# Optimization experiments

Measured on AMD Instinct MI355X. Metric: run time of the kernel, lower is better.

The kernel has to match this reference:

```python
import jax, jax.numpy as jnp
import numpy as np

EPS = 1e-3  # BatchNorm eps from module init
N, C_IN, K = 200000, 256, 27
C_MID = C_IN // 4  # bottleneck expansion = 4


def batch_norm(h, gamma, beta):
    # BatchNorm1d in training mode: biased batch stats over the node dim
    mean = jnp.mean(h, axis=0)
    var = jnp.var(h, axis=0)
    return (h - mean) * jax.lax.rsqrt(var + EPS) * gamma + beta


def setup_inputs() -> dict:
    key = jax.random.key(0)
    ks = jax.random.split(key, 8)
    x = jax.random.normal(ks[0], (N, C_IN), dtype=jnp.float32)
    neigh = jax.random.randint(ks[1], (N, K), 0, N)  # 27-neighbor octree table
    # conv weights (no bias; BN follows). Fan-in scaled init.
    W1 = jax.random.normal(ks[2], (C_IN, C_MID), dtype=jnp.float32) / np.sqrt(C_IN)
    W2 = jax.random.normal(ks[3], (K, C_MID, C_MID), dtype=jnp.float32) / np.sqrt(K * C_MID)
    W3 = jax.random.normal(ks[4], (C_MID, C_IN), dtype=jnp.float32) / np.sqrt(C_MID)
    g1 = jnp.ones((C_MID,), jnp.float32); b1 = jnp.zeros((C_MID,), jnp.float32)
    g2 = jnp.ones((C_MID,), jnp.float32); b2 = jnp.zeros((C_MID,), jnp.float32)
    g3 = jnp.ones((C_IN,), jnp.float32); b3 = jnp.zeros((C_IN,), jnp.float32)
    return {"x": x, "neigh": neigh, "depth": 6,
            "W1": W1, "g1": g1, "b1": b1,
            "W2": W2, "g2": g2, "b2": b2,
            "W3": W3, "g3": g3, "b3": b3}


def reference(x, neigh, depth, W1, g1, b1, W2, g2, b2, W3, g3, b3):
    identity = x
    # conv_bn_relu1: 1x1 octree conv -> BN -> ReLU
    h = jax.nn.relu(batch_norm(x @ W1, g1, b1))  # [N, C_MID]
    # conv_bn_relu2: 3x3 octree conv (27-neighbor gather) -> BN -> ReLU
    gathered = h[neigh]                          # [N, 27, C_MID] irregular gather
    h = jnp.einsum('nkc,kcd->nd', gathered, W2)  # [N, C_MID]
    h = jax.nn.relu(batch_norm(h, g2, b2))
    # conv3: 1x1 octree conv back to C_IN, then BN + residual + ReLU
    h = batch_norm(h @ W3, g3, b3)               # [N, C_IN]
    return jax.nn.relu(h + identity)
```

## Files before the change

kernel.cpp:

```cpp
#include <hip/hip_runtime.h>
#include <stdint.h>

#define N_NODES 200000
#define C_INN   256
#define C_MIDD  64
#define KNB     27

typedef unsigned short u16;
typedef __attribute__((ext_vector_type(8))) short short8;
typedef __attribute__((ext_vector_type(4))) float floatx4;

__device__ inline float bf2f(u16 u) {
  union { uint32_t i; float f; } v; v.i = ((uint32_t)u) << 16; return v.f;
}
__device__ inline u16 f2bf(float f) {
  union { float f; uint32_t i; } v; v.f = f;
  uint32_t lsb = (v.i >> 16) & 1u;
  uint32_t r = v.i + 0x7fffu + lsb;
  return (u16)(r >> 16);
}

__global__ void prep_kernel(const float* __restrict__ W1, const float* __restrict__ W2,
                            const float* __restrict__ W3,
                            u16* __restrict__ w1t, u16* __restrict__ w2t,
                            u16* __restrict__ w3t, float* __restrict__ stats) {
  int tid = blockIdx.x * blockDim.x + threadIdx.x;
  int nth = gridDim.x * blockDim.x;
  for (int i = tid; i < 1536; i += nth) stats[i] = 0.f;
  for (int i = tid; i < 256 * 64; i += nth) {
    int d = i >> 8, k = i & 255;
    w1t[i] = f2bf(W1[k * 64 + d]);
  }
  for (int i = tid; i < 27 * 64 * 64; i += nth) {
    int kn = i >> 12, r = i & 4095, d = r >> 6, c = r & 63;
    w2t[i] = f2bf(W2[kn * 4096 + c * 64 + d]);
  }
  for (int i = tid; i < 256 * 64; i += nth) {
    int d = i >> 6, k = i & 63;
    w3t[i] = f2bf(W3[k * 256 + d]);
  }
}

#define PAD1 136
__global__ __launch_bounds__(256) void gemm1_kernel(const float* __restrict__ x,
                                                    const u16* __restrict__ w1t,
                                                    u16* __restrict__ y1) {
  __shared__ u16 Als[64 * PAD1];
  __shared__ u16 Bls[64 * PAD1];
  int t = threadIdx.x;
  long long rowBase = (long long)blockIdx.x * 64;
  int w = t >> 6, lane = t & 63;
  int m = lane & 15, q = lane >> 4;
  floatx4 acc[4] = {};

  for (int kh = 0; kh < 2; kh++) {
    if (kh) __syncthreads();
    #pragma unroll
    for (int j = 0; j < 8; j++) {
      int lin = j * 256 + t;
      int r = lin >> 5, c4 = lin & 31;
      floatx4 v = ((const floatx4*)x)[(rowBase + r) * 64 + kh * 32 + c4];
      ushort4 u;
      u.x = f2bf(v[0]); u.y = f2bf(v[1]); u.z = f2bf(v[2]); u.w = f2bf(v[3]);
      *(ushort4*)&Als[r * PAD1 + c4 * 4] = u;
    }
    #pragma unroll
    for (int j = 0; j < 4; j++) {
      int lin = j * 256 + t;
      int n = lin >> 4, c8 = lin & 15;
      uint4 u = ((const uint4*)w1t)[n * 32 + kh * 16 + c8];
      *(uint4*)&Bls[n * PAD1 + c8 * 8] = u;
    }
    __syncthreads();
    #pragma unroll
    for (int kc = 0; kc < 4; kc++) {
      short8 af = *(const short8*)&Als[(w * 16 + m) * PAD1 + kc * 32 + q * 8];
      #pragma unroll
      for (int tt = 0; tt < 4; tt++) {
        short8 bf = *(const short8*)&Bls[(tt * 16 + m) * PAD1 + kc * 32 + q * 8];
        acc[tt] = __builtin_amdgcn_mfma_f32_16x16x32_bf16(af, bf, acc[tt], 0, 0, 0);
      }
    }
  }
  long long base = rowBase + w * 16;
  #pragma unroll
  for (int tt = 0; tt < 4; tt++)
    #pragma unroll
    for (int r = 0; r < 4; r++)
      y1[(base + q * 4 + r) * 64 + tt * 16 + m] = f2bf(acc[tt][r]);
}

#define PAD2 72
__global__ __launch_bounds__(256) void gemm2_kernel(const u16* __restrict__ h1,
                                                    const int* __restrict__ neigh,
                                                    const u16* __restrict__ w2t,
                                                    u16* __restrict__ y2) {
  __shared__ u16 Als[64 * PAD2];
  __shared__ u16 Bls[64 * PAD2];
  __shared__ int nidx[64 * 27];
  int t = threadIdx.x;
  long long rowBase = (long long)blockIdx.x * 64;
  #pragma unroll
  for (int j = 0; j < 7; j++) {
    int lin = j * 256 + t;
    if (lin < 64 * 27) nidx[lin] = neigh[rowBase * 27 + lin];
  }
  int w = t >> 6, lane = t & 63;
  int m = lane & 15, q = lane >> 4;
  floatx4 acc[4] = {};

  for (int k = 0; k < KNB; k++) {
    __syncthreads();
    #pragma unroll
    for (int j = 0; j < 2; j++) {
      int lin = j * 256 + t;
      int r = lin >> 3, c8 = lin & 7;
      long long src = (long long)nidx[r * 27 + k] * 8 + c8;
      *(uint4*)&Als[r * PAD2 + c8 * 8] = ((const uint4*)h1)[src];
      *(uint4*)&Bls[r * PAD2 + c8 * 8] = ((const uint4*)w2t)[k * 512 + lin];
    }
    __syncthreads();
    #pragma unroll
    for (int kc = 0; kc < 2; kc++) {
      short8 af = *(const short8*)&Als[(w * 16 + m) * PAD2 + kc * 32 + q * 8];
      #pragma unroll
      for (int tt = 0; tt < 4; tt++) {
        short8 bf = *(const short8*)&Bls[(tt * 16 + m) * PAD2 + kc * 32 + q * 8];
        acc[tt] = __builtin_amdgcn_mfma_f32_16x16x32_bf16(af, bf, acc[tt], 0, 0, 0);
      }
    }
  }
  long long base = rowBase + w * 16;
  #pragma unroll
  for (int tt = 0; tt < 4; tt++)
    #pragma unroll
    for (int r = 0; r < 4; r++)
      y2[(base + q * 4 + r) * 64 + tt * 16 + m] = f2bf(acc[tt][r]);
}

#define PAD3 72
__global__ __launch_bounds__(256) void gemm3_kernel(const u16* __restrict__ h2,
                                                    const u16* __restrict__ w3t,
                                                    float* __restrict__ y3) {
  __shared__ u16 Als[64 * PAD3];
  __shared__ u16 Bls[256 * PAD3];
  int t = threadIdx.x;
  long long rowBase = (long long)blockIdx.x * 64;
  #pragma unroll
  for (int j = 0; j < 2; j++) {
    int lin = j * 256 + t;
    int r = lin >> 3, c8 = lin & 7;
    *(uint4*)&Als[r * PAD3 + c8 * 8] = ((const uint4*)h2)[rowBase * 8 + lin];
  }
  #pragma unroll
  for (int j = 0; j < 8; j++) {
    int lin = j * 256 + t;
    int n = lin >> 3, c8 = lin & 7;
    *(uint4*)&Bls[n * PAD3 + c8 * 8] = ((const uint4*)w3t)[lin];
  }
  __syncthreads();
  int w = t >> 6, lane = t & 63;
  int m = lane & 15, q = lane >> 4;
  floatx4 acc[16] = {};
  short8 af0 = *(const short8*)&Als[(w * 16 + m) * PAD3 + q * 8];
  short8 af1 = *(const short8*)&Als[(w * 16 + m) * PAD3 + 32 + q * 8];
  #pragma unroll
  for (int tt = 0; tt < 16; tt++) {
    short8 b0 = *(const short8*)&Bls[(tt * 16 + m) * PAD3 + q * 8];
    short8 b1 = *(const short8*)&Bls[(tt * 16 + m) * PAD3 + 32 + q * 8];
    acc[tt] = __builtin_amdgcn_mfma_f32_16x16x32_bf16(af0, b0, acc[tt], 0, 0, 0);
    acc[tt] = __builtin_amdgcn_mfma_f32_16x16x32_bf16(af1, b1, acc[tt], 0, 0, 0);
  }
  long long base = rowBase + w * 16;
  #pragma unroll
  for (int tt = 0; tt < 16; tt++)
    #pragma unroll
    for (int r = 0; r < 4; r++)
      y3[(base + q * 4 + r) * 256 + tt * 16 + m] = acc[tt][r];
}

template <int C, bool BF>
__global__ __launch_bounds__(256) void stats_kernel(const void* __restrict__ yv,
                                                    float* __restrict__ sums) {
  const int RPB = 256 / C;
  int t = threadIdx.x;
  int c = t % C, rg = t / C;
  float s = 0.f, sq = 0.f;
  for (long long row = (long long)blockIdx.x * RPB + rg; row < N_NODES;
       row += (long long)gridDim.x * RPB) {
    float v = BF ? bf2f(((const u16*)yv)[row * C + c])
                 : ((const float*)yv)[row * C + c];
    s += v; sq += v * v;
  }
  __shared__ float ls[256], lq[256];
  ls[t] = s; lq[t] = sq;
  __syncthreads();
  if (t < C) {
    float S = 0.f, Q = 0.f;
    for (int g = 0; g < RPB; g++) { S += ls[g * C + t]; Q += lq[g * C + t]; }
    atomicAdd(&sums[t], S);
    atomicAdd(&sums[C + t], Q);
  }
}

__global__ void finalize_kernel(const float* __restrict__ sums, const float* __restrict__ g,
                                const float* __restrict__ b, float* __restrict__ ac, int C) {
  int t = threadIdx.x;
  if (t < C) {
    float inv = 1.f / (float)N_NODES;
    float mean = sums[t] * inv;
    float var = sums[C + t] * inv - mean * mean;
    float a = g[t] * rsqrtf(var + 1e-3f);
    ac[t] = a;
    ac[C + t] = b[t] - mean * a;
  }
}

__global__ __launch_bounds__(256) void apply_bn_relu_kernel(u16* __restrict__ y,
                                                            const float* __restrict__ ac) {
  __shared__ float a[64], cc[64];
  int t = threadIdx.x;
  if (t < 64) { a[t] = ac[t]; cc[t] = ac[64 + t]; }
  __syncthreads();
  const long long total = (long long)N_NODES * 64 / 8;
  for (long long i = (long long)blockIdx.x * 256 + t; i < total;
       i += (long long)gridDim.x * 256) {
    uint4 u = ((uint4*)y)[i];
    int c0 = (int)((i & 7) * 8);
    u16* us = (u16*)&u;
    #pragma unroll
    for (int j = 0; j < 8; j++) {
      float v = bf2f(us[j]);
      v = fmaf(a[c0 + j], v, cc[c0 + j]);
      us[j] = f2bf(fmaxf(v, 0.f));
    }
    ((uint4*)y)[i] = u;
  }
}

__global__ __launch_bounds__(256) void epilogue_kernel(float* __restrict__ y3,
                                                       const float* __restrict__ x,
                                                       const float* __restrict__ ac) {
  __shared__ float a[256], cc[256];
  int t = threadIdx.x;
  a[t] = ac[t]; cc[t] = ac[256 + t];
  __syncthreads();
  const long long total = (long long)N_NODES * 256 / 4;
  for (long long i = (long long)blockIdx.x * 256 + t; i < total;
       i += (long long)gridDim.x * 256) {
    floatx4 v = ((floatx4*)y3)[i];
    floatx4 xi = ((const floatx4*)x)[i];
    int c0 = (int)((i & 63) * 4);
    #pragma unroll
    for (int j = 0; j < 4; j++) {
      float r = fmaf(a[c0 + j], v[j], cc[c0 + j]) + xi[j];
      v[j] = fmaxf(r, 0.f);
    }
    ((floatx4*)y3)[i] = v;
  }
}

extern "C" void kernel_launch(void* const* d_in, const int* in_sizes, int n_in,
                              void* d_out, int out_size, void* d_ws, size_t ws_size,
                              hipStream_t stream) {
  (void)in_sizes; (void)n_in; (void)out_size; (void)ws_size;
  const float* x  = (const float*)d_in[0];
  const int* neigh = (const int*)d_in[1];
  const float* W1 = (const float*)d_in[3];
  const float* g1 = (const float*)d_in[4];
  const float* b1 = (const float*)d_in[5];
  const float* W2 = (const float*)d_in[6];
  const float* g2 = (const float*)d_in[7];
  const float* b2 = (const float*)d_in[8];
  const float* W3 = (const float*)d_in[9];
  const float* g3 = (const float*)d_in[10];
  const float* b3 = (const float*)d_in[11];

  char* ws = (char*)d_ws;
  u16* h1  = (u16*)(ws);
  u16* h2  = (u16*)(ws + 25600000LL);
  u16* w1t = (u16*)(ws + 51200000LL);
  u16* w2t = (u16*)(ws + 51232768LL);
  u16* w3t = (u16*)(ws + 51453952LL);
  float* stats = (float*)(ws + 51486720LL);
  float* s1 = stats,        *ac1 = stats + 128;
  float* s2 = stats + 256,  *ac2 = stats + 384;
  float* s3 = stats + 512,  *ac3 = stats + 1024;
  float* y3 = (float*)d_out;

  const int MB = N_NODES / 64;

  prep_kernel<<<256, 256, 0, stream>>>(W1, W2, W3, w1t, w2t, w3t, stats);

  gemm1_kernel<<<MB, 256, 0, stream>>>(x, w1t, h1);
  stats_kernel<64, true><<<1024, 256, 0, stream>>>(h1, s1);
  finalize_kernel<<<1, 256, 0, stream>>>(s1, g1, b1, ac1, 64);
  apply_bn_relu_kernel<<<2048, 256, 0, stream>>>(h1, ac1);

  gemm2_kernel<<<MB, 256, 0, stream>>>(h1, neigh, w2t, h2);
  stats_kernel<64, true><<<1024, 256, 0, stream>>>(h2, s2);
  finalize_kernel<<<1, 256, 0, stream>>>(s2, g2, b2, ac2, 64);
  apply_bn_relu_kernel<<<2048, 256, 0, stream>>>(h2, ac2);

  gemm3_kernel<<<MB, 256, 0, stream>>>(h2, w3t, y3);
  stats_kernel<256, false><<<2048, 256, 0, stream>>>(y3, s3);
  finalize_kernel<<<1, 256, 0, stream>>>(s3, g3, b3, ac3, 256);
  epilogue_kernel<<<4096, 256, 0, stream>>>(y3, x, ac3);
}
```

Measured before the change: 768.8 us.

## Fuse BN stats into GEMMs, derive BN3 stats via Gram matrix, fuse epilogue

Batch statistics are now computed inside gemm1 and gemm2 epilogues, which removes the separate stats passes. BN3 statistics come from a 64x64 Gram matrix of the post-ReLU h2 multiplied through W3, so the fp32 y3 intermediate is never written or re-read. gemm3 applies BN2+ReLU on load and BN3, the residual and ReLU in its epilogue, writing the output once. gemm2 now takes 256-row tiles that read gathered rows directly from global memory instead of staging through LDS. The costs are a bf16-rounded Gram matrix for the variance, float atomics, and aliasing of G over the w1t workspace.

```diff
diff --git a/kernel.cpp b/kernel.cpp
--- a/kernel.cpp
+++ b/kernel.cpp
@@ -2,9 +2,6 @@
 #include <stdint.h>
 
 #define N_NODES 200000
-#define C_INN   256
-#define C_MIDD  64
-#define KNB     27
 
 typedef unsigned short u16;
 typedef __attribute__((ext_vector_type(8))) short short8;
@@ -16,196 +13,81 @@
 __device__ inline u16 f2bf(float f) {
   union { float f; uint32_t i; } v; v.f = f;
   uint32_t lsb = (v.i >> 16) & 1u;
-  uint32_t r = v.i + 0x7fffu + lsb;
-  return (u16)(r >> 16);
-}
+  return (u16)((v.i + 0x7fffu + lsb) >> 16);
+}
+
 
 __global__ void prep_kernel(const float* __restrict__ W1, const float* __restrict__ W2,
                             const float* __restrict__ W3,
                             u16* __restrict__ w1t, u16* __restrict__ w2t,
-                            u16* __restrict__ w3t, float* __restrict__ stats) {
+                            u16* __restrict__ w3t, float* __restrict__ fl) {
   int tid = blockIdx.x * blockDim.x + threadIdx.x;
   int nth = gridDim.x * blockDim.x;
-  for (int i = tid; i < 1536; i += nth) stats[i] = 0.f;
+  for (int i = tid; i < 512; i += nth) fl[i] = 0.f;
   for (int i = tid; i < 256 * 64; i += nth) {
-    int d = i >> 8, k = i & 255;
-    w1t[i] = f2bf(W1[k * 64 + d]);
+    int n = i >> 8, k = i & 255;
+    w1t[i] = f2bf(W1[k * 64 + n]);
   }
   for (int i = tid; i < 27 * 64 * 64; i += nth) {
-    int kn = i >> 12, r = i & 4095, d = r >> 6, c = r & 63;
-    w2t[i] = f2bf(W2[kn * 4096 + c * 64 + d]);
+    int kn = i >> 12, r = i & 4095, n = r >> 6, k = r & 63;
+    w2t[i] = f2bf(W2[kn * 4096 + k * 64 + n]);
   }
   for (int i = tid; i < 256 * 64; i += nth) {
-    int d = i >> 6, k = i & 63;
-    w3t[i] = f2bf(W3[k * 256 + d]);
-  }
-}
-
-#define PAD1 136
+    int n = i >> 6, k = i & 63;
+    w3t[i] = f2bf(W3[k * 256 + n]);
+  }
+}
+
 __global__ __launch_bounds__(256) void gemm1_kernel(const float* __restrict__ x,
                                                     const u16* __restrict__ w1t,
-                                                    u16* __restrict__ y1) {
-  __shared__ u16 Als[64 * PAD1];
-  __shared__ u16 Bls[64 * PAD1];
+                                                    u16* __restrict__ y1,
+                                                    float* __restrict__ s1) {
+  __shared__ float ps[4][64], pq[4][64];
+  int t = threadIdx.x, w = t >> 6, lane = t & 63, m = lane & 15, q = lane >> 4;
+  long long rowA = (long long)blockIdx.x * 64 + w * 16 + m;
+  const float* xr = x + rowA * 256 + q * 8;
+  floatx4 acc[4] = {};
+  #pragma unroll
+  for (int kc = 0; kc < 8; kc++) {
+    floatx4 v0 = *(const floatx4*)(xr + kc * 32);
+    floatx4 v1 = *(const floatx4*)(xr + kc * 32 + 4);
+    short8 af;
+    af[0] = f2bf(v0[0]); af[1] = f2bf(v0[1]); af[2] = f2bf(v0[2]); af[3] = f2bf(v0[3]);
+    af[4] = f2bf(v1[0]); af[5] = f2bf(v1[1]); af[6] = f2bf(v1[2]); af[7] = f2bf(v1[3]);
+    #pragma unroll
+    for (int tt = 0; tt < 4; tt++) {
+      short8 bf = *(const short8*)(w1t + (tt * 16 + m) * 256 + kc * 32 + q * 8);
+      acc[tt] = __builtin_amdgcn_mfma_f32_16x16x32_bf16(af, bf, acc[tt], 0, 0, 0);
+    }
+  }
+  long long rowC = (long long)blockIdx.x * 64 + w * 16 + q * 4;
+  #pragma unroll
+  for (int tt = 0; tt < 4; tt++) {
+    float s = 0.f, sq = 0.f;
+    #pragma unroll
+    for (int r = 0; r < 4; r++) {
+      float v = acc[tt][r];
+      s += v; sq += v * v;
+      y1[(rowC + r) * 64 + tt * 16 + m] = f2bf(v);
+    }
+    s += __shfl_xor(s, 16); s += __shfl_xor(s, 32);
+    sq += __shfl_xor(sq, 16); sq += __shfl_xor(sq, 32);
+    if (q == 0) { ps[w][tt * 16 + m] = s; pq[w][tt * 16 + m] = sq; }
+  }
+  __syncthreads();
+  if (t < 64) {
+    float S = ps[0][t] + ps[1][t] + ps[2][t] + ps[3][t];
+    float Q = pq[0][t] + pq[1][t] + pq[2][t] + pq[3][t];
+    atomicAdd(&s1[t], S);
+    atomicAdd(&s1[64 + t], Q);
+  }
+}
+
+__global__ void finalize_kernel(const float* __restrict__ sums, const float* __restrict__ g,
+                                const float* __restrict__ b, float* __restrict__ ac, int C,
+                                float* __restrict__ zp, int zn) {
   int t = threadIdx.x;
-  long long rowBase = (long long)blockIdx.x * 64;
-  int w = t >> 6, lane = t & 63;
-  int m = lane & 15, q = lane >> 4;
-  floatx4 acc[4] = {};
-
-  for (int kh = 0; kh < 2; kh++) {
-    if (kh) __syncthreads();
-    #pragma unroll
-    for (int j = 0; j < 8; j++) {
-      int lin = j * 256 + t;
-      int r = lin >> 5, c4 = lin & 31;
-      floatx4 v = ((const floatx4*)x)[(rowBase + r) * 64 + kh * 32 + c4];
-      ushort4 u;
-      u.x = f2bf(v[0]); u.y = f2bf(v[1]); u.z = f2bf(v[2]); u.w = f2bf(v[3]);
-      *(ushort4*)&Als[r * PAD1 + c4 * 4] = u;
-    }
-    #pragma unroll
-    for (int j = 0; j < 4; j++) {
-      int lin = j * 256 + t;
-      int n = lin >> 4, c8 = lin & 15;
-      uint4 u = ((const uint4*)w1t)[n * 32 + kh * 16 + c8];
-      *(uint4*)&Bls[n * PAD1 + c8 * 8] = u;
-    }
-    __syncthreads();
-    #pragma unroll
-    for (int kc = 0; kc < 4; kc++) {
-      short8 af = *(const short8*)&Als[(w * 16 + m) * PAD1 + kc * 32 + q * 8];
-      #pragma unroll
-      for (int tt = 0; tt < 4; tt++) {
-        short8 bf = *(const short8*)&Bls[(tt * 16 + m) * PAD1 + kc * 32 + q * 8];
-        acc[tt] = __builtin_amdgcn_mfma_f32_16x16x32_bf16(af, bf, acc[tt], 0, 0, 0);
-      }
-    }
-  }
-  long long base = rowBase + w * 16;
-  #pragma unroll
-  for (int tt = 0; tt < 4; tt++)
-    #pragma unroll
-    for (int r = 0; r < 4; r++)
-      y1[(base + q * 4 + r) * 64 + tt * 16 + m] = f2bf(acc[tt][r]);
-}
-
-#define PAD2 72
-__global__ __launch_bounds__(256) void gemm2_kernel(const u16* __restrict__ h1,
-                                                    const int* __restrict__ neigh,
-                                                    const u16* __restrict__ w2t,
-                                                    u16* __restrict__ y2) {
-  __shared__ u16 Als[64 * PAD2];
-  __shared__ u16 Bls[64 * PAD2];
-  __shared__ int nidx[64 * 27];
-  int t = threadIdx.x;
-  long long rowBase = (long long)blockIdx.x * 64;
-  #pragma unroll
-  for (int j = 0; j < 7; j++) {
-    int lin = j * 256 + t;
-    if (lin < 64 * 27) nidx[lin] = neigh[rowBase * 27 + lin];
-  }
-  int w = t >> 6, lane = t & 63;
-  int m = lane & 15, q = lane >> 4;
-  floatx4 acc[4] = {};
-
-  for (int k = 0; k < KNB; k++) {
-    __syncthreads();
-    #pragma unroll
-    for (int j = 0; j < 2; j++) {
-      int lin = j * 256 + t;
-      int r = lin >> 3, c8 = lin & 7;
-      long long src = (long long)nidx[r * 27 + k] * 8 + c8;
-      *(uint4*)&Als[r * PAD2 + c8 * 8] = ((const uint4*)h1)[src];
-      *(uint4*)&Bls[r * PAD2 + c8 * 8] = ((const uint4*)w2t)[k * 512 + lin];
-    }
-    __syncthreads();
-    #pragma unroll
-    for (int kc = 0; kc < 2; kc++) {
-      short8 af = *(const short8*)&Als[(w * 16 + m) * PAD2 + kc * 32 + q * 8];
-      #pragma unroll
-      for (int tt = 0; tt < 4; tt++) {
-        short8 bf = *(const short8*)&Bls[(tt * 16 + m) * PAD2 + kc * 32 + q * 8];
-        acc[tt] = __builtin_amdgcn_mfma_f32_16x16x32_bf16(af, bf, acc[tt], 0, 0, 0);
-      }
-    }
-  }
-  long long base = rowBase + w * 16;
-  #pragma unroll
-  for (int tt = 0; tt < 4; tt++)
-    #pragma unroll
-    for (int r = 0; r < 4; r++)
-      y2[(base + q * 4 + r) * 64 + tt * 16 + m] = f2bf(acc[tt][r]);
-}
-
-#define PAD3 72
-__global__ __launch_bounds__(256) void gemm3_kernel(const u16* __restrict__ h2,
-                                                    const u16* __restrict__ w3t,
-                                                    float* __restrict__ y3) {
-  __shared__ u16 Als[64 * PAD3];
-  __shared__ u16 Bls[256 * PAD3];
-  int t = threadIdx.x;
-  long long rowBase = (long long)blockIdx.x * 64;
-  #pragma unroll
-  for (int j = 0; j < 2; j++) {
-    int lin = j * 256 + t;
-    int r = lin >> 3, c8 = lin & 7;
-    *(uint4*)&Als[r * PAD3 + c8 * 8] = ((const uint4*)h2)[rowBase * 8 + lin];
-  }
-  #pragma unroll
-  for (int j = 0; j < 8; j++) {
-    int lin = j * 256 + t;
-    int n = lin >> 3, c8 = lin & 7;
-    *(uint4*)&Bls[n * PAD3 + c8 * 8] = ((const uint4*)w3t)[lin];
-  }
-  __syncthreads();
-  int w = t >> 6, lane = t & 63;
-  int m = lane & 15, q = lane >> 4;
-  floatx4 acc[16] = {};
-  short8 af0 = *(const short8*)&Als[(w * 16 + m) * PAD3 + q * 8];
-  short8 af1 = *(const short8*)&Als[(w * 16 + m) * PAD3 + 32 + q * 8];
-  #pragma unroll
-  for (int tt = 0; tt < 16; tt++) {
-    short8 b0 = *(const short8*)&Bls[(tt * 16 + m) * PAD3 + q * 8];
-    short8 b1 = *(const short8*)&Bls[(tt * 16 + m) * PAD3 + 32 + q * 8];
-    acc[tt] = __builtin_amdgcn_mfma_f32_16x16x32_bf16(af0, b0, acc[tt], 0, 0, 0);
-    acc[tt] = __builtin_amdgcn_mfma_f32_16x16x32_bf16(af1, b1, acc[tt], 0, 0, 0);
-  }
-  long long base = rowBase + w * 16;
-  #pragma unroll
-  for (int tt = 0; tt < 16; tt++)
-    #pragma unroll
-    for (int r = 0; r < 4; r++)
-      y3[(base + q * 4 + r) * 256 + tt * 16 + m] = acc[tt][r];
-}
-
-template <int C, bool BF>
-__global__ __launch_bounds__(256) void stats_kernel(const void* __restrict__ yv,
-                                                    float* __restrict__ sums) {
-  const int RPB = 256 / C;
-  int t = threadIdx.x;
-  int c = t % C, rg = t / C;
-  float s = 0.f, sq = 0.f;
-  for (long long row = (long long)blockIdx.x * RPB + rg; row < N_NODES;
-       row += (long long)gridDim.x * RPB) {
-    float v = BF ? bf2f(((const u16*)yv)[row * C + c])
-                 : ((const float*)yv)[row * C + c];
-    s += v; sq += v * v;
-  }
-  __shared__ float ls[256], lq[256];
-  ls[t] = s; lq[t] = sq;
-  __syncthreads();
-  if (t < C) {
-    float S = 0.f, Q = 0.f;
-    for (int g = 0; g < RPB; g++) { S += ls[g * C + t]; Q += lq[g * C + t]; }
-    atomicAdd(&sums[t], S);
-    atomicAdd(&sums[C + t], Q);
-  }
-}
-
-__global__ void finalize_kernel(const float* __restrict__ sums, const float* __restrict__ g,
-                                const float* __restrict__ b, float* __restrict__ ac, int C) {
-  int t = threadIdx.x;
+  for (int i = t; i < zn; i += blockDim.x) zp[i] = 0.f;
   if (t < C) {
     float inv = 1.f / (float)N_NODES;
     float mean = sums[t] * inv;
@@ -230,33 +112,215 @@
     u16* us = (u16*)&u;
     #pragma unroll
     for (int j = 0; j < 8; j++) {
-      float v = bf2f(us[j]);
-      v = fmaf(a[c0 + j], v, cc[c0 + j]);
+      float v = fmaf(a[c0 + j], bf2f(us[j]), cc[c0 + j]);
       us[j] = f2bf(fmaxf(v, 0.f));
     }
     ((uint4*)y)[i] = u;
   }
 }
 
-__global__ __launch_bounds__(256) void epilogue_kernel(float* __restrict__ y3,
-                                                       const float* __restrict__ x,
-                                                       const float* __restrict__ ac) {
-  __shared__ float a[256], cc[256];
+__global__ __launch_bounds__(256) void gemm2_kernel(const u16* __restrict__ h1,
+                                                    const int* __restrict__ neigh,
+                                                    const u16* __restrict__ w2t,
+                                                    u16* __restrict__ y2,
+                                                    float* __restrict__ s2) {
+  __shared__ int nidx[256 * 27];
+  __shared__ float ps[4][64], pq[4][64];
   int t = threadIdx.x;
-  a[t] = ac[t]; cc[t] = ac[256 + t];
-  __syncthreads();
-  const long long total = (long long)N_NODES * 256 / 4;
-  for (long long i = (long long)blockIdx.x * 256 + t; i < total;
-       i += (long long)gridDim.x * 256) {
-    floatx4 v = ((floatx4*)y3)[i];
-    floatx4 xi = ((const floatx4*)x)[i];
-    int c0 = (int)((i & 63) * 4);
-    #pragma unroll
-    for (int j = 0; j < 4; j++) {
-      float r = fmaf(a[c0 + j], v[j], cc[c0 + j]) + xi[j];
-      v[j] = fmaxf(r, 0.f);
-    }
-    ((floatx4*)y3)[i] = v;
+  long long rowBase = (long long)blockIdx.x * 256;
+  int limit = (int)((N_NODES - rowBase) * 27); if (limit > 6912) limit = 6912;
+  #pragma unroll
+  for (int j = 0; j < 27; j++) {
+    int lin = j * 256 + t;
+    nidx[lin] = (lin < limit) ? neigh[rowBase * 27 + lin] : 0;
+  }
+  __syncthreads();
+  int w = t >> 6, lane = t & 63, m = lane & 15, q = lane >> 4;
+  int rA[4]; bool vA[4];
+  #pragma unroll
+  for (int mt = 0; mt < 4; mt++) {
+    rA[mt] = w * 64 + mt * 16 + m;
+    vA[mt] = (rowBase + rA[mt]) < N_NODES;
+  }
+  floatx4 acc[4][4] = {};
+  for (int k = 0; k < 27; k++) {
+    #pragma unroll
+    for (int kc = 0; kc < 2; kc++) {
+      short8 af[4];
+      #pragma unroll
+      for (int mt = 0; mt < 4; mt++) {
+        int idx = nidx[rA[mt] * 27 + k];
+        uint4 u = *((const uint4*)(h1 + (long long)idx * 64 + kc * 32 + q * 8));
+        if (!vA[mt]) { u.x = 0u; u.y = 0u; u.z = 0u; u.w = 0u; }
+        af[mt] = *(short8*)&u;
+      }
+      #pragma unroll
+      for (int tt = 0; tt < 4; tt++) {
+        short8 bf = *(const short8*)(w2t + k * 4096 + (tt * 16 + m) * 64 + kc * 32 + q * 8);
+        #pragma unroll
+        for (int mt = 0; mt < 4; mt++)
+          acc[mt][tt] = __builtin_amdgcn_mfma_f32_16x16x32_bf16(af[mt], bf, acc[mt][tt], 0, 0, 0);
+      }
+    }
+  }
+  #pragma unroll
+  for (int tt = 0; tt < 4; tt++) {
+    float s = 0.f, sq = 0.f;
+    #pragma unroll
+    for (int mt = 0; mt < 4; mt++) {
+      long long rowC = rowBase + w * 64 + mt * 16 + q * 4;
+      #pragma unroll
+      for (int r = 0; r < 4; r++) {
+        float v = acc[mt][tt][r];
+        s += v; sq += v * v;
+        if (rowC + r < N_NODES) y2[(rowC + r) * 64 + tt * 16 + m] = f2bf(v);
+      }
+    }
+    s += __shfl_xor(s, 16); s += __shfl_xor(s, 32);
+    sq += __shfl_xor(sq, 16); sq += __shfl_xor(sq, 32);
+    if (q == 0) { ps[w][tt * 16 + m] = s; pq[w][tt * 16 + m] = sq; }
+  }
+  __syncthreads();
+  if (t < 64) {
+    float S = ps[0][t] + ps[1][t] + ps[2][t] + ps[3][t];
+    float Q = pq[0][t] + pq[1][t] + pq[2][t] + pq[3][t];
+    atomicAdd(&s2[t], S);
+    atomicAdd(&s2[64 + t], Q);
+  }
+}
+
+__global__ __launch_bounds__(256) void gram_kernel(const u16* __restrict__ y2,
+                                                   const float* __restrict__ ac2,
+                                                   float* __restrict__ G,
+                                                   float* __restrict__ cs) {
+  __shared__ float T[64][130];
+  __shared__ float sld[64];
+  int t = threadIdx.x;
+  if (t < 64) sld[t] = 0.f;
+  __syncthreads();
+  long long nodeBase = (long long)blockIdx.x * 128;
+  int ch0 = (t & 7) * 8;
+  float av[8], cv[8];
+  #pragma unroll
+  for (int j = 0; j < 8; j++) { av[j] = ac2[ch0 + j]; cv[j] = ac2[64 + ch0 + j]; }
+  float myS[8] = {};
+  #pragma unroll
+  for (int i = 0; i < 4; i++) {
+    int node = i * 32 + (t >> 3);
+    long long gn = nodeBase + node;
+    uint4 u = {0u, 0u, 0u, 0u};
+    bool valid = gn < N_NODES;
+    if (valid) u = *((const uint4*)(y2 + gn * 64) + (t & 7));
+    u16* us = (u16*)&u;
+    #pragma unroll
+    for (int j = 0; j < 8; j++) {
+      float v = valid ? fmaxf(fmaf(av[j], bf2f(us[j]), cv[j]), 0.f) : 0.f;
+      T[ch0 + j][node] = v;
+      myS[j] += v;
+    }
+  }
+  #pragma unroll
+  for (int j = 0; j < 8; j++) atomicAdd(&sld[ch0 + j], myS[j]);
+  __syncthreads();
+  int w = t >> 6, lane = t & 63, m = lane & 15, q = lane >> 4;
+  floatx4 gacc[4] = {};
+  #pragma unroll
+  for (int kc = 0; kc < 4; kc++) {
+    short8 af;
+    #pragma unroll
+    for (int j = 0; j < 8; j++) af[j] = f2bf(T[w * 16 + m][kc * 32 + q * 8 + j]);
+    #pragma unroll
+    for (int nt = 0; nt < 4; nt++) {
+      short8 bf;
+      #pragma unroll
+      for (int j = 0; j < 8; j++) bf[j] = f2bf(T[nt * 16 + m][kc * 32 + q * 8 + j]);
+      gacc[nt] = __builtin_amdgcn_mfma_f32_16x16x32_bf16(af, bf, gacc[nt], 0, 0, 0);
+    }
+  }
+  #pragma unroll
+  for (int nt = 0; nt < 4; nt++)
+    #pragma unroll
+    for (int r = 0; r < 4; r++)
+      atomicAdd(&G[(w * 16 + q * 4 + r) * 64 + nt * 16 + m], gacc[nt][r]);
+  if (t < 64) atomicAdd(&cs[t], sld[t]);
+}
+
+__global__ void finalize3_kernel(const float* __restrict__ G, const float* __restrict__ cs,
+                                 const float* __restrict__ W3, const float* __restrict__ g3,
+                                 const float* __restrict__ b3, float* __restrict__ ac3) {
+  __shared__ float Gl[64 * 65];
+  __shared__ float wc[64];
+  int j = threadIdx.x;
+  int c = blockIdx.x;
+  for (int i = 0; i < 64; i++) Gl[i * 65 + j] = G[i * 64 + j];
+  wc[j] = W3[j * 256 + c];
+  __syncthreads();
+  float wjc = wc[j];
+  float mj = 0.f;
+  #pragma unroll 8
+  for (int k = 0; k < 64; k++) mj = fmaf(Gl[j * 65 + k], wc[k], mj);
+  float p = wjc * mj;
+  float ms = cs[j] * wjc;
+  #pragma unroll
+  for (int off = 32; off > 0; off >>= 1) { p += __shfl_xor(p, off); ms += __shfl_xor(ms, off); }
+  if (j == 0) {
+    float inv = 1.f / (float)N_NODES;
+    float mean = ms * inv;
+    float var = p * inv - mean * mean;
+    float a = g3[c] * rsqrtf(var + 1e-3f);
+    ac3[c] = a;
+    ac3[256 + c] = b3[c] - mean * a;
+  }
+}
+
+__global__ __launch_bounds__(256) void gemm3_kernel(const u16* __restrict__ y2,
+                                                    const float* __restrict__ ac2,
+                                                    const u16* __restrict__ w3t,
+                                                    const float* __restrict__ x,
+                                                    const float* __restrict__ ac3,
+                                                    float* __restrict__ out) {
+  int t = threadIdx.x, w = t >> 6, lane = t & 63, m = lane & 15, q = lane >> 4;
+  long long rowBase = (long long)blockIdx.x * 64;
+  floatx4 acc[4][4] = {};
+  #pragma unroll
+  for (int kc = 0; kc < 2; kc++) {
+    float a2v[8], c2v[8];
+    #pragma unroll
+    for (int j = 0; j < 8; j++) {
+      a2v[j] = ac2[kc * 32 + q * 8 + j];
+      c2v[j] = ac2[64 + kc * 32 + q * 8 + j];
+    }
+    short8 af[4];
+    #pragma unroll
+    for (int mt = 0; mt < 4; mt++) {
+      long long row = rowBase + mt * 16 + m;
+      uint4 u = *((const uint4*)(y2 + row * 64 + kc * 32 + q * 8));
+      u16* us = (u16*)&u;
+      #pragma unroll
+      for (int j = 0; j < 8; j++)
+        af[mt][j] = f2bf(fmaxf(fmaf(a2v[j], bf2f(us[j]), c2v[j]), 0.f));
+    }
+    #pragma unroll
+    for (int tt = 0; tt < 4; tt++) {
+      short8 bf = *(const short8*)(w3t + (w * 64 + tt * 16 + m) * 64 + kc * 32 + q * 8);
+      #pragma unroll
+      for (int mt = 0; mt < 4; mt++)
+        acc[mt][tt] = __builtin_amdgcn_mfma_f32_16x16x32_bf16(af[mt], bf, acc[mt][tt], 0, 0, 0);
+    }
+  }
+  #pragma unroll
+  for (int tt = 0; tt < 4; tt++) {
+    int col = w * 64 + tt * 16 + m;
+    float a3v = ac3[col], c3v = ac3[256 + col];
+    #pragma unroll
+    for (int mt = 0; mt < 4; mt++) {
+      long long row = rowBase + mt * 16 + q * 4;
+      #pragma unroll
+      for (int r = 0; r < 4; r++) {
+        float v = fmaf(a3v, acc[mt][tt][r], c3v) + x[(row + r) * 256 + col];
+        out[(row + r) * 256 + col] = fmaxf(v, 0.f);
+      }
+    }
   }
 }
 
@@ -264,46 +328,43 @@
                               void* d_out, int out_size, void* d_ws, size_t ws_size,
                               hipStream_t stream) {
   (void)in_sizes; (void)n_in; (void)out_size; (void)ws_size;
-  const float* x  = (const float*)d_in[0];
+  const float* x   = (const float*)d_in[0];
   const int* neigh = (const int*)d_in[1];
-  const float* W1 = (const float*)d_in[3];
-  const float* g1 = (const float*)d_in[4];
-  const float* b1 = (const float*)d_in[5];
-  const float* W2 = (const float*)d_in[6];
-  const float* g2 = (const float*)d_in[7];
-  const float* b2 = (const float*)d_in[8];
-  const float* W3 = (const float*)d_in[9];
-  const float* g3 = (const float*)d_in[10];
-  const float* b3 = (const float*)d_in[11];
+  const float* W1  = (const float*)d_in[3];
+  const float* g1  = (const float*)d_in[4];
+  const float* b1  = (const float*)d_in[5];
+  const float* W2  = (const float*)d_in[6];
+  const float* g2  = (const float*)d_in[7];
+  const float* b2  = (const float*)d_in[8];
+  const float* W3  = (const float*)d_in[9];
+  const float* g3  = (const float*)d_in[10];
+  const float* b3  = (const float*)d_in[11];
 
   char* ws = (char*)d_ws;
-  u16* h1  = (u16*)(ws);
-  u16* h2  = (u16*)(ws + 25600000LL);
-  u16* w1t = (u16*)(ws + 51200000LL);
+  u16* y1  = (u16*)(ws);
+  u16* y2  = (u16*)(ws + 25600000LL);
+  u16* w1t   = (u16*)(ws + 51200000LL);
+  float* G   = (float*)(ws + 51200000LL);
+  float* cs  = G + 4096;
+  float* ac3 = G + 4160;
   u16* w2t = (u16*)(ws + 51232768LL);
   u16* w3t = (u16*)(ws + 51453952LL);
-  float* stats = (float*)(ws + 51486720LL);
-  float* s1 = stats,        *ac1 = stats + 128;
-  float* s2 = stats + 256,  *ac2 = stats + 384;
-  float* s3 = stats + 512,  *ac3 = stats + 1024;
-  float* y3 = (float*)d_out;
-
-  const int MB = N_NODES / 64;
-
-  prep_kernel<<<256, 256, 0, stream>>>(W1, W2, W3, w1t, w2t, w3t, stats);
-
-  gemm1_kernel<<<MB, 256, 0, stream>>>(x, w1t, h1);
-  stats_kernel<64, true><<<1024, 256, 0, stream>>>(h1, s1);
-  finalize_kernel<<<1, 256, 0, stream>>>(s1, g1, b1, ac1, 64);
-  apply_bn_relu_kernel<<<2048, 256, 0, stream>>>(h1, ac1);
-
-  gemm2_kernel<<<MB, 256, 0, stream>>>(h1, neigh, w2t, h2);
-  stats_kernel<64, true><<<1024, 256, 0, stream>>>(h2, s2);
-  finalize_kernel<<<1, 256, 0, stream>>>(s2, g2, b2, ac2, 64);
-  apply_bn_relu_kernel<<<2048, 256, 0, stream>>>(h2, ac2);
-
-  gemm3_kernel<<<MB, 256, 0, stream>>>(h2, w3t, y3);
-  stats_kernel<256, false><<<2048, 256, 0, stream>>>(y3, s3);
-  finalize_kernel<<<1, 256, 0, stream>>>(s3, g3, b3, ac3, 256);
-  epilogue_kernel<<<4096, 256, 0, stream>>>(y3, x, ac3);
-}
+  float* fl = (float*)(ws + 51486720LL);
+  float* s1  = fl;        float* ac1 = fl + 128;
+  float* s2  = fl + 256;  float* ac2 = fl + 384;
+  float* out = (float*)d_out;
+
+  prep_kernel<<<256, 256, 0, stream>>>(W1, W2, W3, w1t, w2t, w3t, fl);
+
+  gemm1_kernel<<<3125, 256, 0, stream>>>(x, w1t, y1, s1);
+  finalize_kernel<<<1, 256, 0, stream>>>(s1, g1, b1, ac1, 64, s1, 0);
+  apply_bn_relu_kernel<<<2048, 256, 0, stream>>>(y1, ac1);
+
+  gemm2_kernel<<<782, 256, 0, stream>>>(y1, neigh, w2t, y2, s2);
+  finalize_kernel<<<1, 256, 0, stream>>>(s2, g2, b2, ac2, 64, G, 4160);
+
+  gram_kernel<<<1563, 256, 0, stream>>>(y2, ac2, G, cs);
+  finalize3_kernel<<<256, 64, 0, stream>>>(G, cs, W3, g3, b3, ac3);
+
+  gemm3_kernel<<<3125, 256, 0, stream>>>(y2, ac2, w3t, x, ac3, out);
+}
```

Result: no change. 782.3 us (+1.8%).
